# Performance work log

Hardware: AMD Instinct MI355X
Metric: run time of the kernel (lower is better)

## Reference

```python
import jax, jax.numpy as jnp
import numpy as np

B, N, DIM, H, DH = 4, 1024, 512, 8, 64
INNER = H * DH
LN_EPS = 1e-5


def layernorm(x, g, b):
    m = x.mean(-1, keepdims=True)
    v = jnp.var(x, axis=-1, keepdims=True)
    return (x - m) / jnp.sqrt(v + LN_EPS) * g + b


def setup_inputs() -> dict:
    key = jax.random.key(0)
    ks = jax.random.split(key, 8)
    return {
        "q": jax.random.normal(ks[0], (B, N, DIM), jnp.float32),
        "k": jax.random.normal(ks[1], (B, N, DIM), jnp.float32),
        "v": jax.random.normal(ks[2], (B, N, DIM), jnp.float32),
        "ln_g": jnp.ones((DIM,), jnp.float32),
        "ln_b": jnp.zeros((DIM,), jnp.float32),
        "W_in": jax.random.normal(ks[3], (INNER, DIM), jnp.float32) * 0.02,
        "W_out": jax.random.normal(ks[4], (DIM, INNER), jnp.float32) * 0.02,
        "b_out": jnp.zeros((DIM,), jnp.float32),
        "wp_W1": jax.random.normal(ks[5], (DH, 2 * DH), jnp.float32) * 0.05,
        "wp_b1": jnp.zeros((DH,), jnp.float32),
        "wp_ln_g": jnp.ones((DH,), jnp.float32),
        "wp_ln_b": jnp.zeros((DH,), jnp.float32),
        "wp_W2": jax.random.normal(ks[6], (3, DH), jnp.float32) * 0.05,
        "wp_b2": jnp.zeros((3,), jnp.float32),
    }


def reference(q, k, v, ln_g, ln_b, W_in, W_out, b_out,
              wp_W1, wp_b1, wp_ln_g, wp_ln_b, wp_W2, wp_b2):
    b, n, _ = q.shape

    def proj(t):  # [b, n, dim] -> [h, b, n, d]
        y = layernorm(t, ln_g, ln_b) @ W_in.T
        return y.reshape(b, n, H, DH).transpose(2, 0, 1, 3)

    f_q, f_k, f_v = proj(q), proj(k), proj(v)

    # cosine similarity component: [h, b, n, m]
    dots = jnp.einsum('hbnd,hbmd->hbnm', f_q, f_k)
    qn = jnp.linalg.norm(f_q, axis=-1)  # [h, b, n]
    kn = jnp.linalg.norm(f_k, axis=-1)  # [h, b, m]
    cosine_sim = dots / (qn[..., :, None] * kn[..., None, :])

    # centered covariance component
    q_c = f_q - f_q.mean(-1, keepdims=True)
    k_c = f_k - f_k.mean(-1, keepdims=True)
    cov_component = jnp.einsum('hbnd,hbmd->hbnm', q_c, k_c) / DH

    # variance-product component (outer product of per-row variances, unbiased like torch.var)
    q_var = jnp.var(f_q, axis=-1, ddof=1)  # [h, b, n]
    k_var = jnp.var(f_k, axis=-1, ddof=1)  # [h, b, m]
    var_component = (q_var[..., :, None] * k_var[..., None, :]) / DH

    # dynamic per-head mixing weights
    q_global = f_q.mean(axis=(1, 2))  # [h, d]
    k_global = f_k.mean(axis=(1, 2))  # [h, d]
    feats = jnp.concatenate([q_global, k_global], axis=-1)  # [h, 2d]
    hdn = jax.nn.relu(layernorm(feats @ wp_W1.T + wp_b1, wp_ln_g, wp_ln_b))
    weights = jax.nn.softmax(hdn @ wp_W2.T + wp_b2, axis=-1)  # [h, 3]
    w = weights[:, :, None, None, None]  # [h, 3, 1, 1, 1]

    mixed = w[:, 0] * cosine_sim + w[:, 1] * cov_component + w[:, 2] * var_component
    out = jnp.einsum('hbnm,hbmd->hbnd', mixed, f_v)
    out = out.transpose(1, 2, 0, 3).reshape(b, n, INNER)  # 'h b n d -> b n (h d)'
    return out @ W_out.T + b_out
```

## Files before the change

### kernel.cpp

```cpp
#include <hip/hip_runtime.h>
#include <hip/hip_bf16.h>

#define LN_EPS 1e-5f
typedef __attribute__((ext_vector_type(8))) short short8v;
typedef __attribute__((ext_vector_type(4))) short short4v;
typedef __attribute__((ext_vector_type(4))) float f32x4;
typedef __hip_bfloat16 bf16;

__device__ inline float wred_sum(float v) {
#pragma unroll
  for (int off = 1; off < 64; off <<= 1) v += __shfl_xor(v, off, 64);
  return v;
}
__device__ inline float b2f(short s) {
  return __uint_as_float(((unsigned)(unsigned short)s) << 16);
}
__device__ inline short f2bs(float x) {
  union { bf16 h; short s; } u; u.h = __float2bfloat16(x); return u.s;
}
__device__ inline float rbf(float x) {
  return __bfloat162float(__float2bfloat16(x));
}

__global__ __launch_bounds__(256) void lncvt_kernel(
    const float* __restrict__ q, const float* __restrict__ k,
    const float* __restrict__ v,
    const float* __restrict__ g, const float* __restrict__ bln,
    const float* __restrict__ Wi, const float* __restrict__ Wo,
    bf16* __restrict__ abf, bf16* __restrict__ Wib, bf16* __restrict__ Wob) {
  int bid = blockIdx.x, tid = threadIdx.x;
  if (bid < 3072) {
    int wave = tid >> 6, lane = tid & 63;
    int grow = bid * 4 + wave;
    int tensor = grow >> 12, row = grow & 4095;
    const float* src = tensor == 0 ? q : (tensor == 1 ? k : v);
    const float4* p = (const float4*)(src + (size_t)row * 512 + lane * 8);
    float4 a = p[0], b = p[1];
    float s  = a.x + a.y + a.z + a.w + b.x + b.y + b.z + b.w;
    float ss = a.x*a.x + a.y*a.y + a.z*a.z + a.w*a.w
             + b.x*b.x + b.y*b.y + b.z*b.z + b.w*b.w;
    s = wred_sum(s);
    ss = wred_sum(ss);
    float m = s * (1.f / 512.f);
    float r = rsqrtf(ss * (1.f / 512.f) - m * m + LN_EPS);
    float4 g0 = *(const float4*)(g + lane * 8);
    float4 g1 = *(const float4*)(g + lane * 8 + 4);
    float4 b0 = *(const float4*)(bln + lane * 8);
    float4 b1 = *(const float4*)(bln + lane * 8 + 4);
    short8v t;
    t[0] = f2bs((a.x - m) * r * g0.x + b0.x);
    t[1] = f2bs((a.y - m) * r * g0.y + b0.y);
    t[2] = f2bs((a.z - m) * r * g0.z + b0.z);
    t[3] = f2bs((a.w - m) * r * g0.w + b0.w);
    t[4] = f2bs((b.x - m) * r * g1.x + b1.x);
    t[5] = f2bs((b.y - m) * r * g1.y + b1.y);
    t[6] = f2bs((b.z - m) * r * g1.z + b1.z);
    t[7] = f2bs((b.w - m) * r * g1.w + b1.w);
    *(short8v*)(abf + (size_t)grow * 512 + lane * 8) = t;
  } else {
    int e0 = ((bid - 3072) * 256 + tid) * 8;
    float4 a = *(const float4*)(Wi + e0);
    float4 b = *(const float4*)(Wi + e0 + 4);
    short8v t;
    t[0] = f2bs(a.x); t[1] = f2bs(a.y); t[2] = f2bs(a.z); t[3] = f2bs(a.w);
    t[4] = f2bs(b.x); t[5] = f2bs(b.y); t[6] = f2bs(b.z); t[7] = f2bs(b.w);
    *(short8v*)(Wib + e0) = t;
    a = *(const float4*)(Wo + e0);
    b = *(const float4*)(Wo + e0 + 4);
    t[0] = f2bs(a.x); t[1] = f2bs(a.y); t[2] = f2bs(a.z); t[3] = f2bs(a.w);
    t[4] = f2bs(b.x); t[5] = f2bs(b.y); t[6] = f2bs(b.z); t[7] = f2bs(b.w);
    *(short8v*)(Wob + e0) = t;
  }
}

__global__ __launch_bounds__(256) void proj_kernel(
    const bf16* __restrict__ Asrc, const bf16* __restrict__ Wb,
    bf16* __restrict__ f_q, bf16* __restrict__ fkt,
    bf16* __restrict__ fvt,
    float* __restrict__ rn, float* __restrict__ mn, float* __restrict__ vr,
    float* __restrict__ gp) {
  __shared__ __attribute__((aligned(16))) bf16 As[2][64 * 64];
  __shared__ __attribute__((aligned(16))) bf16 Bs[2][128 * 64];
  __shared__ float gpbuf[2][128];
  int tid = threadIdx.x;
  int lin = (blockIdx.x & 7) * 96 + (blockIdx.x >> 3);
  int bi = lin >> 2, bj = lin & 3;
  int row0 = bi * 64;
  int wv = tid >> 6, l = tid & 63, fr = l & 15, lq = l >> 4;
  int wr = wv >> 1, wc = wv & 1;
  f32x4 acc[2][4];
#pragma unroll
  for (int a = 0; a < 2; ++a)
#pragma unroll
    for (int j = 0; j < 4; ++j)
#pragma unroll
      for (int e = 0; e < 4; ++e) acc[a][j][e] = 0.f;

  int swz = (fr & 7) << 4;
  int offA0 = wv * 2048 + l * 16;
  int offB0 = wv * 4096 + l * 16;

#define STAGE(buf, ks)                                                        \
  {                                                                           \
    _Pragma("unroll")                                                         \
    for (int c = 0; c < 2; ++c) {                                             \
      int off = offA0 + c * 1024;                                             \
      int ar = off >> 7;                                                      \
      int sc = (off & 127) ^ ((ar & 7) << 4);                                 \
      const char* gsrc = (const char*)(Asrc + (size_t)(row0 + ar) * 512 + (ks)) + sc; \
      __builtin_amdgcn_global_load_lds(gsrc, (char*)As[buf] + wv * 2048 + c * 1024, 16, 0, 0); \
    }                                                                         \
    _Pragma("unroll")                                                         \
    for (int c = 0; c < 4; ++c) {                                             \
      int off = offB0 + c * 1024;                                             \
      int br = off >> 7;                                                      \
      int sc = (off & 127) ^ ((br & 7) << 4);                                 \
      const char* gsrc = (const char*)(Wb + (size_t)(bj * 128 + br) * 512 + (ks)) + sc; \
      __builtin_amdgcn_global_load_lds(gsrc, (char*)Bs[buf] + wv * 4096 + c * 1024, 16, 0, 0); \
    }                                                                         \
  }

  STAGE(0, 0);
#pragma unroll
  for (int t = 0; t < 8; ++t) {
    int cur = t & 1;
    if (t < 7) {
      STAGE(cur ^ 1, (t + 1) * 64);
      asm volatile("s_waitcnt vmcnt(6)" ::: "memory");
    } else {
      asm volatile("s_waitcnt vmcnt(0)" ::: "memory");
    }
    __builtin_amdgcn_s_barrier();
#pragma unroll
    for (int kk = 0; kk < 64; kk += 32) {
      int csw = (kk * 2 + lq * 16) ^ swz;
      short8v a0 = *(const short8v*)&As[cur][(wr * 32 + fr) * 64 + (csw >> 1)];
      short8v a1 = *(const short8v*)&As[cur][(wr * 32 + 16 + fr) * 64 + (csw >> 1)];
#pragma unroll
      for (int j = 0; j < 4; ++j) {
        short8v bv = *(const short8v*)&Bs[cur][(wc * 64 + j * 16 + fr) * 64 + (csw >> 1)];
        acc[0][j] = __builtin_amdgcn_mfma_f32_16x16x32_bf16(a0, bv, acc[0][j], 0, 0, 0);
        acc[1][j] = __builtin_amdgcn_mfma_f32_16x16x32_bf16(a1, bv, acc[1][j], 0, 0, 0);
      }
    }
    __builtin_amdgcn_s_barrier();
  }
#undef STAGE

  int tensor = bi >> 6, rb = bi & 63;
  int b = rb >> 4, n0 = (rb & 15) * 64;
  int h = bj * 2 + wc, hb = h * 4 + b;
  if (tensor == 2) {
#pragma unroll
    for (int a = 0; a < 2; ++a) {
      int m0l = n0 + wr * 32 + a * 16 + lq * 4;
#pragma unroll
      for (int j = 0; j < 4; ++j) {
        int dv = j * 16 + fr;
        short4v t;
#pragma unroll
        for (int rr = 0; rr < 4; ++rr) t[rr] = f2bs(acc[a][j][rr]);
        *(short4v*)(fvt + (size_t)(hb * 64 + dv) * 1024 + m0l) = t;
      }
    }
    return;
  }
  float vb[2][4][4];
#pragma unroll
  for (int a = 0; a < 2; ++a)
#pragma unroll
    for (int j = 0; j < 4; ++j)
#pragma unroll
      for (int rr = 0; rr < 4; ++rr) vb[a][j][rr] = rbf(acc[a][j][rr]);

#pragma unroll
  for (int a = 0; a < 2; ++a) {
    float sr[4], s2[4];
#pragma unroll
    for (int rr = 0; rr < 4; ++rr) {
      float s = 0.f, ss = 0.f;
#pragma unroll
      for (int j = 0; j < 4; ++j) {
        float x = vb[a][j][rr];
        s += x; ss += x * x;
      }
#pragma unroll
      for (int off = 1; off < 16; off <<= 1) {
        s += __shfl_xor(s, off, 64);
        ss += __shfl_xor(ss, off, 64);
      }
      sr[rr] = s; s2[rr] = ss;
    }
    int nbase = n0 + wr * 32 + a * 16 + lq * 4;
    if (tensor == 0) {
#pragma unroll
      for (int j = 0; j < 4; ++j) {
        int d = j * 16 + fr;
#pragma unroll
        for (int rr = 0; rr < 4; ++rr)
          f_q[(size_t)(b * 1024 + nbase + rr) * 512 + h * 64 + d] =
              __float2bfloat16(acc[a][j][rr]);
      }
      if (fr == 0)
#pragma unroll
        for (int rr = 0; rr < 4; ++rr) {
          size_t idx = (size_t)hb * 1024 + nbase + rr;
          float mean = sr[rr] * (1.f / 64.f);
          rn[idx] = rsqrtf(s2[rr]);
          mn[idx] = mean;
          vr[idx] = (s2[rr] - 64.f * mean * mean) * (1.f / 63.f);
        }
    } else {
#pragma unroll
      for (int j = 0; j < 4; ++j) {
        int dk = j * 16 + fr;
        short4v tp;
#pragma unroll
        for (int rr = 0; rr < 4; ++rr) tp[rr] = f2bs(acc[a][j][rr]);
        *(short4v*)(fkt + (size_t)(hb * 64 + dk) * 1024 + nbase) = tp;
      }
      if (fr == 0)
#pragma unroll
        for (int rr = 0; rr < 4; ++rr) {
          size_t idx = 32768 + (size_t)hb * 1024 + nbase + rr;
          float mean = sr[rr] * (1.f / 64.f);
          mn[idx] = mean;
          vr[idx] = (s2[rr] - 64.f * mean * mean) * (1.f / 63.f);
        }
    }
  }
#pragma unroll
  for (int j = 0; j < 4; ++j) {
    float c = 0.f;
#pragma unroll
    for (int a = 0; a < 2; ++a)
#pragma unroll
      for (int rr = 0; rr < 4; ++rr) c += vb[a][j][rr];
    c += __shfl_xor(c, 16, 64);
    c += __shfl_xor(c, 32, 64);
    if (lq == 0) gpbuf[wr][wc * 64 + j * 16 + fr] = c;
  }
  __syncthreads();
  if (tid < 128)
    gp[(size_t)(tensor * 64 + rb) * 512 + bj * 128 + tid] =
        gpbuf[0][tid] + gpbuf[1][tid];
}

__global__ __launch_bounds__(256) void outproj_kernel(
    const bf16* __restrict__ Ab, const bf16* __restrict__ Wb,
    const float* __restrict__ bias, float* __restrict__ out) {
  __shared__ __attribute__((aligned(16))) bf16 As[2][64 * 64];
  __shared__ __attribute__((aligned(16))) bf16 Bs[2][128 * 64];
  int tid = threadIdx.x;
  int lin = (blockIdx.x & 7) * 32 + (blockIdx.x >> 3);
  int bi = lin >> 2, bj = lin & 3;
  int row0 = bi * 64;
  int wv = tid >> 6, l = tid & 63, fr = l & 15, lq = l >> 4;
  int wr = wv >> 1, wc = wv & 1;
  f32x4 acc[2][4];
#pragma unroll
  for (int a = 0; a < 2; ++a)
#pragma unroll
    for (int j = 0; j < 4; ++j)
#pragma unroll
      for (int e = 0; e < 4; ++e) acc[a][j][e] = 0.f;

  int swz = (fr & 7) << 4;
  int offA0 = wv * 2048 + l * 16;
  int offB0 = wv * 4096 + l * 16;

#define STAGE(buf, ks)                                                        \
  {                                                                           \
    _Pragma("unroll")                                                         \
    for (int c = 0; c < 2; ++c) {                                             \
      int off = offA0 + c * 1024;                                             \
      int ar = off >> 7;                                                      \
      int sc = (off & 127) ^ ((ar & 7) << 4);                                 \
      const char* gsrc = (const char*)(Ab + (size_t)(row0 + ar) * 512 + (ks)) + sc; \
      __builtin_amdgcn_global_load_lds(gsrc, (char*)As[buf] + wv * 2048 + c * 1024, 16, 0, 0); \
    }                                                                         \
    _Pragma("unroll")                                                         \
    for (int c = 0; c < 4; ++c) {                                             \
      int off = offB0 + c * 1024;                                             \
      int br = off >> 7;                                                      \
      int sc = (off & 127) ^ ((br & 7) << 4);                                 \
      const char* gsrc = (const char*)(Wb + (size_t)(bj * 128 + br) * 512 + (ks)) + sc; \
      __builtin_amdgcn_global_load_lds(gsrc, (char*)Bs[buf] + wv * 4096 + c * 1024, 16, 0, 0); \
    }                                                                         \
  }

  STAGE(0, 0);
#pragma unroll
  for (int t = 0; t < 8; ++t) {
    int cur = t & 1;
    if (t < 7) {
      STAGE(cur ^ 1, (t + 1) * 64);
      asm volatile("s_waitcnt vmcnt(6)" ::: "memory");
    } else {
      asm volatile("s_waitcnt vmcnt(0)" ::: "memory");
    }
    __builtin_amdgcn_s_barrier();
#pragma unroll
    for (int kk = 0; kk < 64; kk += 32) {
      int csw = (kk * 2 + lq * 16) ^ swz;
      short8v a0 = *(const short8v*)&As[cur][(wr * 32 + fr) * 64 + (csw >> 1)];
      short8v a1 = *(const short8v*)&As[cur][(wr * 32 + 16 + fr) * 64 + (csw >> 1)];
#pragma unroll
      for (int j = 0; j < 4; ++j) {
        short8v bv = *(const short8v*)&Bs[cur][(wc * 64 + j * 16 + fr) * 64 + (csw >> 1)];
        acc[0][j] = __builtin_amdgcn_mfma_f32_16x16x32_bf16(a0, bv, acc[0][j], 0, 0, 0);
        acc[1][j] = __builtin_amdgcn_mfma_f32_16x16x32_bf16(a1, bv, acc[1][j], 0, 0, 0);
      }
    }
    __builtin_amdgcn_s_barrier();
  }
#undef STAGE
#pragma unroll
  for (int a = 0; a < 2; ++a)
#pragma unroll
    for (int j = 0; j < 4; ++j) {
      int col = bj * 128 + wc * 64 + j * 16 + fr;
      float bvv = bias[col];
#pragma unroll
      for (int rr = 0; rr < 4; ++rr)
        out[(size_t)(row0 + wr * 32 + a * 16 + lq * 4 + rr) * 512 + col] =
            acc[a][j][rr] + bvv;
    }
}

__global__ __launch_bounds__(256) void aux_kernel(
    const bf16* __restrict__ fvt, const bf16* __restrict__ fkt,
    const float* __restrict__ mn, const float* __restrict__ vr,
    const float* __restrict__ gp,
    const float* __restrict__ W1, const float* __restrict__ b1,
    const float* __restrict__ lg, const float* __restrict__ lb,
    const float* __restrict__ W2, const float* __restrict__ b2,
    float* __restrict__ part, float* __restrict__ kvm, float* __restrict__ kvv,
    float* __restrict__ wts) {
  __shared__ float sh[2560];
  int bid = blockIdx.x, tid = threadIdx.x;
  int wv = tid >> 6, l = tid & 63, fr = l & 15, lq = l >> 4;
  if (bid < 128) {
    int hb = bid >> 2, mc = bid & 3;
    f32x4 apl[4], aht[4];
#pragma unroll
    for (int j = 0; j < 4; ++j)
#pragma unroll
      for (int e = 0; e < 4; ++e) { apl[j][e] = 0.f; aht[j][e] = 0.f; }
    size_t arow = (size_t)(hb * 64 + wv * 16 + fr) * 1024;
#pragma unroll 2
    for (int m0 = 0; m0 < 256; m0 += 32) {
      size_t moff = mc * 256 + m0 + lq * 8;
      const float* mnp = mn + 32768 + (size_t)hb * 1024 + moff;
      const float* vrp = vr + 32768 + (size_t)hb * 1024 + moff;
      float4 mv0 = *(const float4*)mnp;
      float4 mv1 = *(const float4*)(mnp + 4);
      float4 vv0 = *(const float4*)vrp;
      float4 vv1 = *(const float4*)(vrp + 4);
      float rnv[8];
      rnv[0] = rsqrtf(63.f * vv0.x + 64.f * mv0.x * mv0.x);
      rnv[1] = rsqrtf(63.f * vv0.y + 64.f * mv0.y * mv0.y);
      rnv[2] = rsqrtf(63.f * vv0.z + 64.f * mv0.z * mv0.z);
      rnv[3] = rsqrtf(63.f * vv0.w + 64.f * mv0.w * mv0.w);
      rnv[4] = rsqrtf(63.f * vv1.x + 64.f * mv1.x * mv1.x);
      rnv[5] = rsqrtf(63.f * vv1.y + 64.f * mv1.y * mv1.y);
      rnv[6] = rsqrtf(63.f * vv1.z + 64.f * mv1.z * mv1.z);
      rnv[7] = rsqrtf(63.f * vv1.w + 64.f * mv1.w * mv1.w);
      short8v av = *(const short8v*)(fvt + arow + moff);
#pragma unroll
      for (int j = 0; j < 4; ++j) {
        size_t brow = (size_t)(hb * 64 + j * 16 + fr) * 1024 + moff;
        short8v bp = *(const short8v*)(fkt + brow);
        short8v bh;
#pragma unroll
        for (int e = 0; e < 8; ++e) bh[e] = f2bs(b2f(bp[e]) * rnv[e]);
        apl[j] = __builtin_amdgcn_mfma_f32_16x16x32_bf16(av, bp, apl[j], 0, 0, 0);
        aht[j] = __builtin_amdgcn_mfma_f32_16x16x32_bf16(av, bh, aht[j], 0, 0, 0);
      }
    }
    size_t base = (size_t)(hb * 4 + mc) * 8192;
#pragma unroll
    for (int j = 0; j < 4; ++j)
#pragma unroll
      for (int rr = 0; rr < 4; ++rr) {
        int dv = wv * 16 + lq * 4 + rr, dk = j * 16 + fr;
        part[base + dv * 64 + dk] = apl[j][rr];
        part[base + 4096 + dv * 64 + dk] = aht[j][rr];
      }
  } else if (bid < 160) {
    int hb = bid - 128;
    float* kmL = sh; float* kvL = sh + 1024; float* red = sh + 2048;
    for (int i = tid; i < 1024; i += 256) {
      kmL[i] = mn[32768 + hb * 1024 + i];
      kvL[i] = vr[32768 + hb * 1024 + i];
    }
    __syncthreads();
    int dv = tid >> 2, seg = tid & 3;
    float am = 0.f, av = 0.f;
    size_t rowb = (size_t)(hb * 64 + dv) * 1024 + seg * 256;
    for (int i = 0; i < 256; i += 8) {
      short8v vv = *(const short8v*)(fvt + rowb + i);
#pragma unroll
      for (int e = 0; e < 8; ++e) {
        float f = b2f(vv[e]);
        am += kmL[seg * 256 + i + e] * f;
        av += kvL[seg * 256 + i + e] * f;
      }
    }
    red[dv * 4 + seg] = am;
    red[256 + dv * 4 + seg] = av;
    __syncthreads();
    if (tid < 64) {
      kvm[hb * 64 + tid] = red[tid * 4] + red[tid * 4 + 1] + red[tid * 4 + 2] + red[tid * 4 + 3];
      kvv[hb * 64 + tid] = red[256 + tid * 4] + red[256 + tid * 4 + 1] +
                           red[256 + tid * 4 + 2] + red[256 + tid * 4 + 3];
    }
  } else {
    int h = bid - 160;
    float* red = sh;
    float* fqv = sh + 512;
    float* fkv = sh + 576;
    float* pred = sh + 640;
    int cl = tid & 63, part4 = tid >> 6;
    float sq = 0.f, sk = 0.f;
#pragma unroll
    for (int p = 0; p < 16; ++p) {
      sq += gp[(size_t)(part4 * 16 + p) * 512 + h * 64 + cl];
      sk += gp[(size_t)(64 + part4 * 16 + p) * 512 + h * 64 + cl];
    }
    red[part4 * 128 + cl] = sq;
    red[part4 * 128 + 64 + cl] = sk;
    __syncthreads();
    if (tid < 128) {
      float vsum = red[tid] + red[128 + tid] + red[256 + tid] + red[384 + tid];
      if (tid < 64) fqv[tid] = vsum * (1.f / 4096.f);
      else          fkv[tid - 64] = vsum * (1.f / 4096.f);
    }
    __syncthreads();
    int j = tid & 63;
    float pp = 0.f;
#pragma unroll
    for (int i = 0; i < 16; ++i) {
      pp += fqv[part4 * 16 + i] * W1[j * 128 + part4 * 16 + i];
      pp += fkv[part4 * 16 + i] * W1[j * 128 + 64 + part4 * 16 + i];
    }
    pred[part4 * 64 + j] = pp;
    __syncthreads();
    if (tid < 64) {
      float pre = b1[j] + pred[j] + pred[64 + j] + pred[128 + j] + pred[192 + j];
      float s = wred_sum(pre);
      float ss = wred_sum(pre * pre);
      float mean = s * (1.f / 64.f);
      float var = ss * (1.f / 64.f) - mean * mean;
      float hdn = (pre - mean) * rsqrtf(var + LN_EPS) * lg[j] + lb[j];
      hdn = fmaxf(hdn, 0.f);
      float l0 = wred_sum(hdn * W2[0 * 64 + j]) + b2[0];
      float l1 = wred_sum(hdn * W2[1 * 64 + j]) + b2[1];
      float l2 = wred_sum(hdn * W2[2 * 64 + j]) + b2[2];
      float mx = fmaxf(l0, fmaxf(l1, l2));
      float e0 = __expf(l0 - mx), e1 = __expf(l1 - mx), e2 = __expf(l2 - mx);
      float inv = 1.f / (e0 + e1 + e2);
      if (j == 0) {
        wts[h * 3 + 0] = e0 * inv;
        wts[h * 3 + 1] = e1 * inv;
        wts[h * 3 + 2] = e2 * inv;
      }
    }
  }
}

__global__ __launch_bounds__(256) void apply_kernel(
    const bf16* __restrict__ f_q, const float* __restrict__ Gpart,
    const float* __restrict__ rn, const float* __restrict__ mn,
    const float* __restrict__ vr, const float* __restrict__ wts,
    const float* __restrict__ kvm, const float* __restrict__ kvv,
    bf16* __restrict__ attnb) {
  __shared__ bf16 Qs[64 * 72];
  __shared__ bf16 Ap[64 * 72];
  __shared__ bf16 Ah[64 * 72];
  __shared__ float qrnL[64], qmnL[64], qvrL[64], kvmL[64], kvvL[64];
  int lin = (blockIdx.x & 7) * 64 + (blockIdx.x >> 3);
  int hbid = lin >> 4, qt = lin & 15;
  int h = hbid >> 2, b = hbid & 3;
  int tid = threadIdx.x;
  int wv = tid >> 6, l = tid & 63, fr = l & 15, lq = l >> 4;
  {
    int row = tid >> 2, qq = (tid & 3) * 16;
    const bf16* qsrc = f_q + (size_t)(b * 1024 + qt * 64 + row) * 512 + h * 64 + qq;
    *(short8v*)&Qs[row * 72 + qq] = *(const short8v*)qsrc;
    *(short8v*)&Qs[row * 72 + qq + 8] = *(const short8v*)(qsrc + 8);
    const float* psrc = Gpart + (size_t)hbid * 32768 + row * 64 + qq;
#pragma unroll
    for (int c = 0; c < 4; ++c) {
      float4 spl = {0.f, 0.f, 0.f, 0.f}, sht = {0.f, 0.f, 0.f, 0.f};
#pragma unroll
      for (int mc = 0; mc < 4; ++mc) {
        float4 p = *(const float4*)(psrc + mc * 8192 + c * 4);
        float4 t = *(const float4*)(psrc + mc * 8192 + 4096 + c * 4);
        spl.x += p.x; spl.y += p.y; spl.z += p.z; spl.w += p.w;
        sht.x += t.x; sht.y += t.y; sht.z += t.z; sht.w += t.w;
      }
      Ap[row * 72 + qq + c * 4 + 0] = __float2bfloat16(spl.x);
      Ap[row * 72 + qq + c * 4 + 1] = __float2bfloat16(spl.y);
      Ap[row * 72 + qq + c * 4 + 2] = __float2bfloat16(spl.z);
      Ap[row * 72 + qq + c * 4 + 3] = __float2bfloat16(spl.w);
      Ah[row * 72 + qq + c * 4 + 0] = __float2bfloat16(sht.x);
      Ah[row * 72 + qq + c * 4 + 1] = __float2bfloat16(sht.y);
      Ah[row * 72 + qq + c * 4 + 2] = __float2bfloat16(sht.z);
      Ah[row * 72 + qq + c * 4 + 3] = __float2bfloat16(sht.w);
    }
  }
  if (tid < 64) {
    qrnL[tid] = rn[(size_t)hbid * 1024 + qt * 64 + tid];
    qmnL[tid] = mn[(size_t)hbid * 1024 + qt * 64 + tid];
    qvrL[tid] = vr[(size_t)hbid * 1024 + qt * 64 + tid];
    kvmL[tid] = kvm[hbid * 64 + tid];
    kvvL[tid] = kvv[hbid * 64 + tid];
  }
  __syncthreads();
  f32x4 ap_[4], ah_[4];
#pragma unroll
  for (int j = 0; j < 4; ++j)
#pragma unroll
    for (int e = 0; e < 4; ++e) { ap_[j][e] = 0.f; ah_[j][e] = 0.f; }
#pragma unroll
  for (int kk = 0; kk < 64; kk += 32) {
    short8v aq = *(const short8v*)&Qs[(wv * 16 + fr) * 72 + kk + lq * 8];
#pragma unroll
    for (int j = 0; j < 4; ++j) {
      short8v bp = *(const short8v*)&Ap[(j * 16 + fr) * 72 + kk + lq * 8];
      short8v bh = *(const short8v*)&Ah[(j * 16 + fr) * 72 + kk + lq * 8];
      ap_[j] = __builtin_amdgcn_mfma_f32_16x16x32_bf16(aq, bp, ap_[j], 0, 0, 0);
      ah_[j] = __builtin_amdgcn_mfma_f32_16x16x32_bf16(aq, bh, ah_[j], 0, 0, 0);
    }
  }
  float w0 = wts[h * 3 + 0], w1 = wts[h * 3 + 1], w2 = wts[h * 3 + 2];
  float f1 = w1 * (1.f / 64.f), w264 = w2 * (1.f / 64.f);
#pragma unroll
  for (int j = 0; j < 4; ++j) {
    int dv = j * 16 + fr;
    float km = kvmL[dv], kv2 = kvvL[dv];
#pragma unroll
    for (int rr = 0; rr < 4; ++rr) {
      int n = wv * 16 + lq * 4 + rr;
      float o = w0 * qrnL[n] * ah_[j][rr] + f1 * ap_[j][rr]
              - w1 * qmnL[n] * km + w264 * qvrL[n] * kv2;
      attnb[(size_t)(b * 1024 + qt * 64 + n) * 512 + h * 64 + dv] = __float2bfloat16(o);
    }
  }
}

extern "C" void kernel_launch(void* const* d_in, const int* in_sizes, int n_in,
                              void* d_out, int out_size, void* d_ws, size_t ws_size,
                              hipStream_t stream) {
  const float* q     = (const float*)d_in[0];
  const float* k     = (const float*)d_in[1];
  const float* v     = (const float*)d_in[2];
  const float* ln_g  = (const float*)d_in[3];
  const float* ln_b  = (const float*)d_in[4];
  const float* W_in  = (const float*)d_in[5];
  const float* W_out = (const float*)d_in[6];
  const float* b_out = (const float*)d_in[7];
  const float* wp_W1 = (const float*)d_in[8];
  const float* wp_b1 = (const float*)d_in[9];
  const float* wp_lg = (const float*)d_in[10];
  const float* wp_lb = (const float*)d_in[11];
  const float* wp_W2 = (const float*)d_in[12];
  const float* wp_b2 = (const float*)d_in[13];
  float* out = (float*)d_out;

  char* w8 = (char*)d_ws;
  bf16* abf   = (bf16*)(w8);
  float* Gpart = (float*)(w8);
  bf16* f_q   = (bf16*)(w8 + (12u << 20));
  bf16* fkt   = (bf16*)(w8 + (16u << 20));
  bf16* fvt   = (bf16*)(w8 + (24u << 20));
  bf16* attnb = (bf16*)(w8 + (28u << 20));
  bf16* Wib   = (bf16*)(w8 + (32u << 20));
  bf16* Wob   = (bf16*)(w8 + (32u << 20) + (512u << 10));
  float* fb   = (float*)(w8 + (33u << 20));
  float* rn  = fb;
  float* mn  = fb + 32768;
  float* vr  = fb + 98304;
  float* gp  = fb + 163840;
  float* kvm = fb + 229376;
  float* kvv = fb + 231424;
  float* wts = fb + 233472;

  lncvt_kernel<<<3200, 256, 0, stream>>>(q, k, v, ln_g, ln_b, W_in, W_out,
                                         abf, Wib, Wob);
  proj_kernel<<<768, 256, 0, stream>>>(
      abf, Wib, f_q, fkt, fvt, rn, mn, vr, gp);
  aux_kernel<<<168, 256, 0, stream>>>(
      fvt, fkt, mn, vr, gp, wp_W1, wp_b1, wp_lg, wp_lb, wp_W2, wp_b2,
      Gpart, kvm, kvv, wts);
  apply_kernel<<<512, 256, 0, stream>>>(
      f_q, Gpart, rn, mn, vr, wts, kvm, kvv, attnb);
  outproj_kernel<<<256, 256, 0, stream>>>(attnb, Wob, b_out, out);
}
```

Before: 59.88 us.

## Fuse input layernorm into projection GEMM and fold LN affine into weights

Moves the layernorm of q/k/v into the projection GEMM: each block computes per-row mean/rstd, then normalizes and converts fp32 activations to bf16 while staging tiles into LDS. The LN gain is folded into W_in during weight conversion and the LN bias becomes a per-output bias vector added after accumulation, so the intermediate bf16 activation buffer and its write/read round-trip disappear. In exchange, each of the four column blocks sharing a row block recomputes its row statistics and re-reads fp32 inputs, and the double-buffered async LDS pipeline is replaced by a single buffer with two full barriers per k-step, which can expose memory latency.

```diff
diff --git a/kernel.cpp b/kernel.cpp
--- a/kernel.cpp
+++ b/kernel.cpp
@@ -22,72 +22,85 @@
   return __bfloat162float(__float2bfloat16(x));
 }
 
-__global__ __launch_bounds__(256) void lncvt_kernel(
+__global__ __launch_bounds__(256) void wcvt_kernel(
+    const float* __restrict__ Wi, const float* __restrict__ Wo,
+    const float* __restrict__ g, const float* __restrict__ bln,
+    bf16* __restrict__ Wib, bf16* __restrict__ Wob, float* __restrict__ cb) {
+  int bid = blockIdx.x, tid = threadIdx.x;
+  if (bid < 128) {
+    int e0 = (bid * 256 + tid) * 8;
+    int d0 = e0 & 511;
+    float4 a = *(const float4*)(Wi + e0);
+    float4 b = *(const float4*)(Wi + e0 + 4);
+    float4 ga = *(const float4*)(g + d0);
+    float4 gb = *(const float4*)(g + d0 + 4);
+    short8v t;
+    t[0] = f2bs(a.x * ga.x); t[1] = f2bs(a.y * ga.y);
+    t[2] = f2bs(a.z * ga.z); t[3] = f2bs(a.w * ga.w);
+    t[4] = f2bs(b.x * gb.x); t[5] = f2bs(b.y * gb.y);
+    t[6] = f2bs(b.z * gb.z); t[7] = f2bs(b.w * gb.w);
+    *(short8v*)(Wib + e0) = t;
+    a = *(const float4*)(Wo + e0);
+    b = *(const float4*)(Wo + e0 + 4);
+    t[0] = f2bs(a.x); t[1] = f2bs(a.y); t[2] = f2bs(a.z); t[3] = f2bs(a.w);
+    t[4] = f2bs(b.x); t[5] = f2bs(b.y); t[6] = f2bs(b.z); t[7] = f2bs(b.w);
+    *(short8v*)(Wob + e0) = t;
+  } else {
+    int o = (bid - 128) * 64 + (tid >> 2);
+    int seg = tid & 3;
+    const float* wr_ = Wi + (size_t)o * 512 + seg * 128;
+    const float* br_ = bln + seg * 128;
+    float s = 0.f;
+#pragma unroll 8
+    for (int i = 0; i < 32; ++i) {
+      float4 w4 = *(const float4*)(wr_ + i * 4);
+      float4 b4 = *(const float4*)(br_ + i * 4);
+      s += w4.x * b4.x + w4.y * b4.y + w4.z * b4.z + w4.w * b4.w;
+    }
+    s += __shfl_xor(s, 1, 64);
+    s += __shfl_xor(s, 2, 64);
+    if (seg == 0) cb[o] = s;
+  }
+}
+
+__global__ __launch_bounds__(256) void proj_kernel(
     const float* __restrict__ q, const float* __restrict__ k,
-    const float* __restrict__ v,
-    const float* __restrict__ g, const float* __restrict__ bln,
-    const float* __restrict__ Wi, const float* __restrict__ Wo,
-    bf16* __restrict__ abf, bf16* __restrict__ Wib, bf16* __restrict__ Wob) {
-  int bid = blockIdx.x, tid = threadIdx.x;
-  if (bid < 3072) {
-    int wave = tid >> 6, lane = tid & 63;
-    int grow = bid * 4 + wave;
-    int tensor = grow >> 12, row = grow & 4095;
-    const float* src = tensor == 0 ? q : (tensor == 1 ? k : v);
-    const float4* p = (const float4*)(src + (size_t)row * 512 + lane * 8);
+    const float* __restrict__ v, const bf16* __restrict__ Wb,
+    const float* __restrict__ cb,
+    bf16* __restrict__ f_q, bf16* __restrict__ fkt,
+    bf16* __restrict__ fvt,
+    float* __restrict__ rn, float* __restrict__ mn, float* __restrict__ vr,
+    float* __restrict__ gp) {
+  __shared__ __attribute__((aligned(16))) bf16 As[64 * 64];
+  __shared__ __attribute__((aligned(16))) bf16 Bs[128 * 64];
+  __shared__ float gpbuf[2][128];
+  __shared__ float lmS[64], lrS[64];
+  int tid = threadIdx.x;
+  int lin = (blockIdx.x & 7) * 96 + (blockIdx.x >> 3);
+  int bi = lin >> 2, bj = lin & 3;
+  int tensor = bi >> 6, rb = bi & 63;
+  const float* A = tensor == 0 ? q : (tensor == 1 ? k : v);
+  int row0 = rb * 64;
+  int wv = tid >> 6, l = tid & 63, fr = l & 15, lq = l >> 4;
+  int wr = wv >> 1, wc = wv & 1;
+
+  for (int r_ = 0; r_ < 16; ++r_) {
+    int row = wv * 16 + r_;
+    const float4* p = (const float4*)(A + (size_t)(row0 + row) * 512 + l * 8);
     float4 a = p[0], b = p[1];
     float s  = a.x + a.y + a.z + a.w + b.x + b.y + b.z + b.w;
     float ss = a.x*a.x + a.y*a.y + a.z*a.z + a.w*a.w
              + b.x*b.x + b.y*b.y + b.z*b.z + b.w*b.w;
     s = wred_sum(s);
     ss = wred_sum(ss);
-    float m = s * (1.f / 512.f);
-    float r = rsqrtf(ss * (1.f / 512.f) - m * m + LN_EPS);
-    float4 g0 = *(const float4*)(g + lane * 8);
-    float4 g1 = *(const float4*)(g + lane * 8 + 4);
-    float4 b0 = *(const float4*)(bln + lane * 8);
-    float4 b1 = *(const float4*)(bln + lane * 8 + 4);
-    short8v t;
-    t[0] = f2bs((a.x - m) * r * g0.x + b0.x);
-    t[1] = f2bs((a.y - m) * r * g0.y + b0.y);
-    t[2] = f2bs((a.z - m) * r * g0.z + b0.z);
-    t[3] = f2bs((a.w - m) * r * g0.w + b0.w);
-    t[4] = f2bs((b.x - m) * r * g1.x + b1.x);
-    t[5] = f2bs((b.y - m) * r * g1.y + b1.y);
-    t[6] = f2bs((b.z - m) * r * g1.z + b1.z);
-    t[7] = f2bs((b.w - m) * r * g1.w + b1.w);
-    *(short8v*)(abf + (size_t)grow * 512 + lane * 8) = t;
-  } else {
-    int e0 = ((bid - 3072) * 256 + tid) * 8;
-    float4 a = *(const float4*)(Wi + e0);
-    float4 b = *(const float4*)(Wi + e0 + 4);
-    short8v t;
-    t[0] = f2bs(a.x); t[1] = f2bs(a.y); t[2] = f2bs(a.z); t[3] = f2bs(a.w);
-    t[4] = f2bs(b.x); t[5] = f2bs(b.y); t[6] = f2bs(b.z); t[7] = f2bs(b.w);
-    *(short8v*)(Wib + e0) = t;
-    a = *(const float4*)(Wo + e0);
-    b = *(const float4*)(Wo + e0 + 4);
-    t[0] = f2bs(a.x); t[1] = f2bs(a.y); t[2] = f2bs(a.z); t[3] = f2bs(a.w);
-    t[4] = f2bs(b.x); t[5] = f2bs(b.y); t[6] = f2bs(b.z); t[7] = f2bs(b.w);
-    *(short8v*)(Wob + e0) = t;
-  }
-}
-
-__global__ __launch_bounds__(256) void proj_kernel(
-    const bf16* __restrict__ Asrc, const bf16* __restrict__ Wb,
-    bf16* __restrict__ f_q, bf16* __restrict__ fkt,
-    bf16* __restrict__ fvt,
-    float* __restrict__ rn, float* __restrict__ mn, float* __restrict__ vr,
-    float* __restrict__ gp) {
-  __shared__ __attribute__((aligned(16))) bf16 As[2][64 * 64];
-  __shared__ __attribute__((aligned(16))) bf16 Bs[2][128 * 64];
-  __shared__ float gpbuf[2][128];
-  int tid = threadIdx.x;
-  int lin = (blockIdx.x & 7) * 96 + (blockIdx.x >> 3);
-  int bi = lin >> 2, bj = lin & 3;
-  int row0 = bi * 64;
-  int wv = tid >> 6, l = tid & 63, fr = l & 15, lq = l >> 4;
-  int wr = wv >> 1, wc = wv & 1;
+    if (l == 0) {
+      float m = s * (1.f / 512.f);
+      lmS[row] = m;
+      lrS[row] = rsqrtf(ss * (1.f / 512.f) - m * m + LN_EPS);
+    }
+  }
+  __syncthreads();
+
   f32x4 acc[2][4];
 #pragma unroll
   for (int a = 0; a < 2; ++a)
@@ -97,57 +110,59 @@
       for (int e = 0; e < 4; ++e) acc[a][j][e] = 0.f;
 
   int swz = (fr & 7) << 4;
-  int offA0 = wv * 2048 + l * 16;
   int offB0 = wv * 4096 + l * 16;
 
-#define STAGE(buf, ks)                                                        \
-  {                                                                           \
-    _Pragma("unroll")                                                         \
-    for (int c = 0; c < 2; ++c) {                                             \
-      int off = offA0 + c * 1024;                                             \
-      int ar = off >> 7;                                                      \
-      int sc = (off & 127) ^ ((ar & 7) << 4);                                 \
-      const char* gsrc = (const char*)(Asrc + (size_t)(row0 + ar) * 512 + (ks)) + sc; \
-      __builtin_amdgcn_global_load_lds(gsrc, (char*)As[buf] + wv * 2048 + c * 1024, 16, 0, 0); \
-    }                                                                         \
-    _Pragma("unroll")                                                         \
-    for (int c = 0; c < 4; ++c) {                                             \
-      int off = offB0 + c * 1024;                                             \
-      int br = off >> 7;                                                      \
-      int sc = (off & 127) ^ ((br & 7) << 4);                                 \
-      const char* gsrc = (const char*)(Wb + (size_t)(bj * 128 + br) * 512 + (ks)) + sc; \
-      __builtin_amdgcn_global_load_lds(gsrc, (char*)Bs[buf] + wv * 4096 + c * 1024, 16, 0, 0); \
-    }                                                                         \
-  }
-
-  STAGE(0, 0);
-#pragma unroll
-  for (int t = 0; t < 8; ++t) {
-    int cur = t & 1;
-    if (t < 7) {
-      STAGE(cur ^ 1, (t + 1) * 64);
-      asm volatile("s_waitcnt vmcnt(6)" ::: "memory");
-    } else {
-      asm volatile("s_waitcnt vmcnt(0)" ::: "memory");
-    }
-    __builtin_amdgcn_s_barrier();
+  for (int ks = 0; ks < 512; ks += 64) {
+#pragma unroll
+    for (int c = 0; c < 2; ++c) {
+      int off = wv * 2048 + c * 1024 + l * 16;
+      int ar = off >> 7;
+      int sc = (off & 127) ^ ((ar & 7) << 4);
+      int col = sc >> 1;
+      const float* src = A + (size_t)(row0 + ar) * 512 + ks + col;
+      float4 x0 = *(const float4*)src;
+      float4 x1 = *(const float4*)(src + 4);
+      float m = lmS[ar], r = lrS[ar];
+      short8v t;
+      t[0] = f2bs((x0.x - m) * r); t[1] = f2bs((x0.y - m) * r);
+      t[2] = f2bs((x0.z - m) * r); t[3] = f2bs((x0.w - m) * r);
+      t[4] = f2bs((x1.x - m) * r); t[5] = f2bs((x1.y - m) * r);
+      t[6] = f2bs((x1.z - m) * r); t[7] = f2bs((x1.w - m) * r);
+      *(short8v*)((char*)As + off) = t;
+    }
+#pragma unroll
+    for (int c = 0; c < 4; ++c) {
+      int off = offB0 + c * 1024;
+      int br = off >> 7;
+      int sc = (off & 127) ^ ((br & 7) << 4);
+      const char* gsrc = (const char*)(Wb + (size_t)(bj * 128 + br) * 512 + ks) + sc;
+      __builtin_amdgcn_global_load_lds(gsrc, (char*)Bs + wv * 4096 + c * 1024, 16, 0, 0);
+    }
+    __syncthreads();
 #pragma unroll
     for (int kk = 0; kk < 64; kk += 32) {
       int csw = (kk * 2 + lq * 16) ^ swz;
-      short8v a0 = *(const short8v*)&As[cur][(wr * 32 + fr) * 64 + (csw >> 1)];
-      short8v a1 = *(const short8v*)&As[cur][(wr * 32 + 16 + fr) * 64 + (csw >> 1)];
+      short8v a0 = *(const short8v*)&As[(wr * 32 + fr) * 64 + (csw >> 1)];
+      short8v a1 = *(const short8v*)&As[(wr * 32 + 16 + fr) * 64 + (csw >> 1)];
 #pragma unroll
       for (int j = 0; j < 4; ++j) {
-        short8v bv = *(const short8v*)&Bs[cur][(wc * 64 + j * 16 + fr) * 64 + (csw >> 1)];
+        short8v bv = *(const short8v*)&Bs[(wc * 64 + j * 16 + fr) * 64 + (csw >> 1)];
         acc[0][j] = __builtin_amdgcn_mfma_f32_16x16x32_bf16(a0, bv, acc[0][j], 0, 0, 0);
         acc[1][j] = __builtin_amdgcn_mfma_f32_16x16x32_bf16(a1, bv, acc[1][j], 0, 0, 0);
       }
     }
-    __builtin_amdgcn_s_barrier();
-  }
-#undef STAGE
-
-  int tensor = bi >> 6, rb = bi & 63;
+    __syncthreads();
+  }
+
+#pragma unroll
+  for (int j = 0; j < 4; ++j) {
+    float cbv = cb[bj * 128 + wc * 64 + j * 16 + fr];
+#pragma unroll
+    for (int a = 0; a < 2; ++a)
+#pragma unroll
+      for (int rr = 0; rr < 4; ++rr) acc[a][j][rr] += cbv;
+  }
+
   int b = rb >> 4, n0 = (rb & 15) * 64;
   int h = bj * 2 + wc, hb = h * 4 + b;
   if (tensor == 2) {
@@ -570,7 +585,6 @@
   float* out = (float*)d_out;
 
   char* w8 = (char*)d_ws;
-  bf16* abf   = (bf16*)(w8);
   float* Gpart = (float*)(w8);
   bf16* f_q   = (bf16*)(w8 + (12u << 20));
   bf16* fkt   = (bf16*)(w8 + (16u << 20));
@@ -586,11 +600,11 @@
   float* kvm = fb + 229376;
   float* kvv = fb + 231424;
   float* wts = fb + 233472;
-
-  lncvt_kernel<<<3200, 256, 0, stream>>>(q, k, v, ln_g, ln_b, W_in, W_out,
-                                         abf, Wib, Wob);
+  float* cb  = fb + 233504;
+
+  wcvt_kernel<<<136, 256, 0, stream>>>(W_in, W_out, ln_g, ln_b, Wib, Wob, cb);
   proj_kernel<<<768, 256, 0, stream>>>(
-      abf, Wib, f_q, fkt, fvt, rn, mn, vr, gp);
+      q, k, v, Wib, cb, f_q, fkt, fvt, rn, mn, vr, gp);
   aux_kernel<<<168, 256, 0, stream>>>(
       fvt, fkt, mn, vr, gp, wp_W1, wp_b1, wp_lg, wp_lb, wp_W2, wp_b2,
       Gpart, kvm, kvv, wts);
```

Measured after the change: 72.47 us. 21.0% more time.
